# Kernel optimization log

Hardware: AMD Instinct MI355X
Metric: run time of the kernel (lower is better)

The kernel has to match this reference:

```python
import jax, jax.numpy as jnp
import numpy as np


def setup_inputs() -> dict:
    key = jax.random.key(0)
    ks = jax.random.split(key, 8)
    B, C, H, W = 4, 256, 64, 64
    C8 = C // 8
    x = jax.random.normal(ks[0], (B, C, H, W), dtype=jnp.float32)
    # 1x1 conv weights as (out_ch, in_ch) matrices + biases
    Wq = jax.random.normal(ks[1], (C8, C), dtype=jnp.float32) * (1.0 / np.sqrt(C))
    bq = jnp.zeros((C8,), dtype=jnp.float32)
    Wk = jax.random.normal(ks[2], (C8, C), dtype=jnp.float32) * (1.0 / np.sqrt(C))
    bk = jnp.zeros((C8,), dtype=jnp.float32)
    Wv = jax.random.normal(ks[3], (C, C), dtype=jnp.float32) * (1.0 / np.sqrt(C))
    bv = jnp.zeros((C,), dtype=jnp.float32)
    gamma = jax.random.normal(ks[4], (1,), dtype=jnp.float32) * 0.1
    return {"x": x, "Wq": Wq, "bq": bq, "Wk": Wk, "bk": bk, "Wv": Wv, "bv": bv, "gamma": gamma}


def reference(x, Wq, bq, Wk, bk, Wv, bv, gamma):
    B, C, H, W = x.shape
    N = H * W
    xf = x.reshape(B, C, N)  # (B, C, N)
    # 1x1 convs == per-pixel channel matmuls
    q = jnp.einsum('oc,bcn->bon', Wq, xf) + bq[None, :, None]  # (B, C8, N)
    k = jnp.einsum('oc,bcn->bon', Wk, xf) + bk[None, :, None]  # (B, C8, N)
    v = jnp.einsum('oc,bcn->bon', Wv, xf) + bv[None, :, None]  # (B, C, N)
    energy = jnp.einsum('bcn,bcm->bnm', q, k)  # (B, N, N)
    attention = jax.nn.softmax(energy, axis=-1)
    # out[b,c,n] = sum_m v[b,c,m] * attention[b,n,m]
    out = jnp.einsum('bcm,bnm->bcn', v, attention)
    out = out.reshape(B, C, H, W)
    return gamma * out + x
```

## Files before the change

kernel.cpp:

```cpp
#include <hip/hip_runtime.h>
#include <hip/hip_bf16.h>
#include <cstddef>
#include <cstdint>

#define CCH 256
#define DQK 32
#define NPX 4096
#define BQ2 128
#define BM  64
#define NB  4

typedef __attribute__((ext_vector_type(8))) short bf16x8;
typedef __attribute__((ext_vector_type(4))) float f32x4;
typedef __attribute__((ext_vector_type(4))) unsigned int u32x4;

#if __has_builtin(__builtin_amdgcn_exp2f)
#define EXP2F(x) __builtin_amdgcn_exp2f(x)
#else
#define EXP2F(x) exp2f(x)
#endif

__device__ inline unsigned short f2bf(float f) {
    unsigned u = __builtin_bit_cast(unsigned, f);
    u += 0x7FFFu + ((u >> 16) & 1u);
    return (unsigned short)(u >> 16);
}
__device__ inline float bf2f(unsigned short h) {
    unsigned u = (unsigned)h << 16;
    return __builtin_bit_cast(float, u);
}
__device__ inline unsigned pkbf(float a, float b) {
    __hip_bfloat162 h = __float22bfloat162_rn(make_float2(a, b));
    unsigned u;
    __builtin_memcpy(&u, &h, 4);
    return u;
}

__global__ __launch_bounds__(256) void convert_kernel(
    const float* __restrict__ Wq, const float* __restrict__ bq,
    const float* __restrict__ Wk, const float* __restrict__ bk,
    const float* __restrict__ Wv, const float* __restrict__ bv,
    unsigned short* __restrict__ Wb, float* __restrict__ bb)
{
    const float LOG2E = 1.4426950408889634f;
    const int o = blockIdx.x;
    const int c = threadIdx.x;
    float v;
    if (o < 32)       v = Wq[o * CCH + c] * LOG2E;
    else if (o < 64)  v = Wk[(o - 32) * CCH + c];
    else              v = Wv[(o - 64) * CCH + c];
    Wb[o * CCH + c] = f2bf(v);
    if (c == 0)
        bb[o] = (o < 32) ? bq[o] * LOG2E : (o < 64) ? bk[o - 32] : bv[o - 64];
}

__global__ __launch_bounds__(512) void proj_mfma(
    const float* __restrict__ x,
    const unsigned short* __restrict__ Wb, const float* __restrict__ bb,
    unsigned short* __restrict__ ws)
{
    __shared__ __align__(16) unsigned short xT[64][264];

    const int tid  = threadIdx.x;
    const int lane = tid & 63;
    const int w    = tid >> 6;
    const int ln   = lane & 15;
    const int g    = lane >> 4;
    const int bid  = blockIdx.x;

    const int xcd  = bid & 7;
    const int idx  = bid >> 3;
    const int slab = xcd + 8 * (idx / 5);
    const int ocg  = idx % 5;
    const int b    = slab >> 6;
    const int pxt  = slab & 63;
    const int pxg0 = pxt * 64;

    const int mt    = w >> 1;
    const int ocrow = ocg * 64 + mt * 16 + ln;
    bf16x8 a[8];
#pragma unroll
    for (int k8 = 0; k8 < 8; ++k8)
        a[k8] = *(const bf16x8*)(Wb + (size_t)ocrow * CCH + k8 * 32 + g * 8);

    {
        const int pxl = (tid & 15) * 4;
        const int c0  = (tid >> 4) * 8;
        float4 xv[8];
#pragma unroll
        for (int cc = 0; cc < 8; ++cc)
            xv[cc] = *(const float4*)(x + ((size_t)(b * CCH + c0 + cc)) * NPX + pxg0 + pxl);
#pragma unroll
        for (int j = 0; j < 4; ++j) {
            unsigned u[4];
#pragma unroll
            for (int h = 0; h < 4; ++h) {
                const float f0 = ((const float*)&xv[2 * h])[j];
                const float f1 = ((const float*)&xv[2 * h + 1])[j];
                u[h] = pkbf(f0, f1);
            }
            *(u32x4*)&xT[pxl + j][c0] = (u32x4){u[0], u[1], u[2], u[3]};
        }
    }
    __syncthreads();

    const int nt0 = (w & 1) * 2;
    const float4 bb4 = *(const float4*)(bb + ocg * 64 + mt * 16 + g * 4);
    f32x4 acc0 = (f32x4){bb4.x, bb4.y, bb4.z, bb4.w};
    f32x4 acc1 = acc0;
#pragma unroll
    for (int k8 = 0; k8 < 8; ++k8) {
        const bf16x8 b0 = *(const bf16x8*)&xT[nt0 * 16 + ln][k8 * 32 + g * 8];
        const bf16x8 b1 = *(const bf16x8*)&xT[nt0 * 16 + 16 + ln][k8 * 32 + g * 8];
        acc0 = __builtin_amdgcn_mfma_f32_16x16x32_bf16(a[k8], b0, acc0, 0, 0, 0);
        acc1 = __builtin_amdgcn_mfma_f32_16x16x32_bf16(a[k8], b1, acc1, 0, 0, 0);
    }

    unsigned short* qT = ws;
    unsigned short* kT = ws + (size_t)NB * NPX * 32;
    unsigned short* vb = ws + (size_t)2 * NB * NPX * 32;
#pragma unroll
    for (int j = 0; j < 2; ++j) {
        const f32x4 acc = j ? acc1 : acc0;
        const int px = pxg0 + (nt0 + j) * 16 + ln;
        if (ocg == 0) {
            const unsigned lo = pkbf(acc[0], acc[1]);
            const unsigned hi = pkbf(acc[2], acc[3]);
            unsigned short* dst = (mt < 2)
                ? qT + ((size_t)b * NPX + px) * 32 + mt * 16 + g * 4
                : kT + ((size_t)b * NPX + px) * 32 + (mt - 2) * 16 + g * 4;
            *(uint2*)dst = make_uint2(lo, hi);
        } else {
            const int c_row = (ocg - 1) * 64 + mt * 16 + g * 4;
#pragma unroll
            for (int rr = 0; rr < 4; ++rr)
                vb[((size_t)(b * CCH + c_row + rr)) * NPX + px] = f2bf(acc[rr]);
        }
    }
}

__global__ __launch_bounds__(512, 4) void attn_kernel(
    const unsigned short* __restrict__ qT, const unsigned short* __restrict__ kT,
    const unsigned short* __restrict__ vB, const float* __restrict__ x,
    const float* __restrict__ gamma, float* __restrict__ out,
    unsigned short* __restrict__ opart, float* __restrict__ mlm,
    float* __restrict__ mll, int ns)
{
    __shared__ __align__(16) unsigned short Pl[2][BQ2 * 64];
    __shared__ float scb[2][BQ2];
    __shared__ int   flg[2][8];
    __shared__ float l_lds[BQ2];

    const int tid  = threadIdx.x;
    const int lane = tid & 63;
    const int w    = tid >> 6;
    const int ln   = lane & 15;
    const int g    = lane >> 4;
    const int bid  = blockIdx.x;

    const int b    = (bid & 7) >> 1;
    const int jb   = ((bid >> 3) << 1) | (bid & 1);
    const int tile = jb / ns;
    const int s    = jb - tile * ns;
    const int n0   = tile * BQ2;

    const bf16x8 qf = *(const bf16x8*)(qT + ((size_t)b * NPX + n0 + w * 16 + ln) * 32 + g * 8);

    f32x4 acc[8][2];
#pragma unroll
    for (int qt = 0; qt < 8; ++qt) {
        acc[qt][0] = (f32x4){0.f, 0.f, 0.f, 0.f};
        acc[qt][1] = (f32x4){0.f, 0.f, 0.f, 0.f};
    }
    float mreg = -INFINITY, lreg = 0.f;

    const unsigned short* kTb = kT + (size_t)b * NPX * 32;
    const unsigned short* vb  = vB + ((size_t)b * CCH + w * 32) * NPX;
    const int kbase = s * (NPX / ns);
    const int iters = NPX / (ns * BM);
    const unsigned swz   = ((unsigned)ln & 7u) << 4;
    const unsigned myrow = (unsigned)(w * 16 + ln) * 128u;
    const float THR2 = 11.544655f;

    for (int t = 0; t < iters; ++t) {
        const int m0 = kbase + t * BM;

        f32x4 e[4];
#pragma unroll
        for (int s4 = 0; s4 < 4; ++s4) {
            const bf16x8 ka = *(const bf16x8*)(kTb + (size_t)(m0 + s4 * 16 + ln) * 32 + g * 8);
            e[s4] = __builtin_amdgcn_mfma_f32_16x16x32_bf16(
                        ka, qf, (f32x4){0.f, 0.f, 0.f, 0.f}, 0, 0, 0);
        }

        float lm = -INFINITY;
#pragma unroll
        for (int s4 = 0; s4 < 4; ++s4)
#pragma unroll
            for (int rr = 0; rr < 4; ++rr) lm = fmaxf(lm, e[s4][rr]);
        lm = fmaxf(lm, __shfl_xor(lm, 16));
        lm = fmaxf(lm, __shfl_xor(lm, 32));
        const float mnew = (lm <= mreg + THR2) ? mreg : lm;
        const float sc   = EXP2F(mreg - mnew);
        float ps = 0.f;
#pragma unroll
        for (int s4 = 0; s4 < 4; ++s4)
#pragma unroll
            for (int rr = 0; rr < 4; ++rr) {
                const float p = EXP2F(e[s4][rr] - mnew);
                e[s4][rr] = p;
                ps += p;
            }
        ps += __shfl_xor(ps, 16);
        ps += __shfl_xor(ps, 32);
        lreg = lreg * sc + ps;
        mreg = mnew;

        const int bw = t & 1;
        char* const pwb = (char*)&Pl[bw][0];
#pragma unroll
        for (int s4 = 0; s4 < 4; ++s4) {
            uint2 pk;
            pk.x = pkbf(e[s4][0], e[s4][1]);
            pk.y = pkbf(e[s4][2], e[s4][3]);
            *(uint2*)(pwb + myrow + (((unsigned)(s4 * 32 + g * 8)) ^ swz)) = pk;
        }
        if (g == 0) scb[bw][w * 16 + ln] = sc;
        const int allsk = __all(sc == 1.0f);
        if (lane == 0) flg[bw][w] = allsk;

        bf16x8 va[2][2];
#pragma unroll
        for (int ct = 0; ct < 2; ++ct) {
            const unsigned short* vrow = vb + (size_t)(ct * 16 + ln) * NPX + m0 + g * 8;
            va[ct][0] = *(const bf16x8*)(vrow);
            va[ct][1] = *(const bf16x8*)(vrow + 32);
        }

        asm volatile("s_waitcnt lgkmcnt(0)" ::: "memory");
        __builtin_amdgcn_s_barrier();

        int sk = flg[bw][0];
#pragma unroll
        for (int i = 1; i < 8; ++i) sk &= flg[bw][i];
        if (!sk) {
#pragma unroll
            for (int qt = 0; qt < 8; ++qt) {
                const float scq = scb[bw][qt * 16 + ln];
#pragma unroll
                for (int rr = 0; rr < 4; ++rr) {
                    acc[qt][0][rr] *= scq;
                    acc[qt][1][rr] *= scq;
                }
            }
        }
#pragma unroll
        for (int qt = 0; qt < 8; ++qt) {
            const unsigned rb = (unsigned)(qt * 16 + ln) * 128u;
            const bf16x8 pf0 = *(const bf16x8*)(pwb + rb + (((unsigned)(g * 16))      ^ swz));
            const bf16x8 pf1 = *(const bf16x8*)(pwb + rb + (((unsigned)(64 + g * 16)) ^ swz));
            acc[qt][0] = __builtin_amdgcn_mfma_f32_16x16x32_bf16(va[0][0], pf0, acc[qt][0], 0, 0, 0);
            acc[qt][0] = __builtin_amdgcn_mfma_f32_16x16x32_bf16(va[0][1], pf1, acc[qt][0], 0, 0, 0);
            acc[qt][1] = __builtin_amdgcn_mfma_f32_16x16x32_bf16(va[1][0], pf0, acc[qt][1], 0, 0, 0);
            acc[qt][1] = __builtin_amdgcn_mfma_f32_16x16x32_bf16(va[1][1], pf1, acc[qt][1], 0, 0, 0);
        }
    }

    if (opart) {
        const size_t sb = (size_t)(s * NB + b);
#pragma unroll
        for (int qt = 0; qt < 8; ++qt)
#pragma unroll
            for (int ct = 0; ct < 2; ++ct) {
                const size_t c0 = sb * CCH + w * 32 + ct * 16 + g * 4;
#pragma unroll
                for (int rr = 0; rr < 4; ++rr)
                    opart[(c0 + rr) * NPX + n0 + qt * 16 + ln] = f2bf(acc[qt][ct][rr]);
            }
        if (g == 0) {
            mlm[sb * NPX + n0 + w * 16 + ln] = mreg;
            mll[sb * NPX + n0 + w * 16 + ln] = lreg;
        }
    } else {
        if (g == 0) l_lds[w * 16 + ln] = lreg;
        __syncthreads();
        const float gm = gamma[0];
#pragma unroll
        for (int qt = 0; qt < 8; ++qt) {
            const float iv = 1.f / l_lds[qt * 16 + ln];
#pragma unroll
            for (int ct = 0; ct < 2; ++ct) {
                const size_t c0 = (size_t)b * CCH + w * 32 + ct * 16 + g * 4;
#pragma unroll
                for (int rr = 0; rr < 4; ++rr) {
                    const size_t idx = (c0 + rr) * NPX + n0 + qt * 16 + ln;
                    out[idx] = gm * acc[qt][ct][rr] * iv + x[idx];
                }
            }
        }
    }
}

__global__ __launch_bounds__(256) void combine_kernel(
    const unsigned short* __restrict__ opart,
    const float* __restrict__ mlm, const float* __restrict__ mll,
    const float* __restrict__ x, const float* __restrict__ gamma,
    float* __restrict__ out, int ns)
{
    const int idx = blockIdx.x * 256 + threadIdx.x;
    const int bc  = idx >> 9;
    const int b   = bc / CCH;
    const int c   = bc - b * CCH;
    const int n0  = (idx & 511) * 8;

    float M[8];
#pragma unroll
    for (int i = 0; i < 8; ++i) M[i] = -INFINITY;
    for (int s = 0; s < ns; ++s) {
        const float* mp = mlm + ((size_t)(s * NB + b)) * NPX + n0;
#pragma unroll
        for (int i = 0; i < 8; ++i) M[i] = fmaxf(M[i], mp[i]);
    }

    float L[8], O[8];
#pragma unroll
    for (int i = 0; i < 8; ++i) { L[i] = 0.f; O[i] = 0.f; }
    for (int s = 0; s < ns; ++s) {
        const size_t sb = (size_t)(s * NB + b);
        const float* mp = mlm + sb * NPX + n0;
        const float* lp = mll + sb * NPX + n0;
        const bf16x8 v8 = *(const bf16x8*)(opart + (sb * CCH + c) * NPX + n0);
#pragma unroll
        for (int i = 0; i < 8; ++i) {
            const float wgt = EXP2F(mp[i] - M[i]);
            L[i] += wgt * lp[i];
            O[i] += wgt * bf2f((unsigned short)v8[i]);
        }
    }

    const float gm = gamma[0];
    const size_t xo = (size_t)bc * NPX + n0;
    float4 r0, r1;
    const float4 x0 = *(const float4*)(x + xo);
    const float4 x1 = *(const float4*)(x + xo + 4);
    r0.x = gm * O[0] / L[0] + x0.x;  r0.y = gm * O[1] / L[1] + x0.y;
    r0.z = gm * O[2] / L[2] + x0.z;  r0.w = gm * O[3] / L[3] + x0.w;
    r1.x = gm * O[4] / L[4] + x1.x;  r1.y = gm * O[5] / L[5] + x1.y;
    r1.z = gm * O[6] / L[6] + x1.z;  r1.w = gm * O[7] / L[7] + x1.w;
    *(float4*)(out + xo)     = r0;
    *(float4*)(out + xo + 4) = r1;
}

extern "C" void kernel_launch(void* const* d_in, const int* in_sizes, int n_in,
                              void* d_out, int out_size, void* d_ws, size_t ws_size,
                              hipStream_t stream)
{
    const float* x  = (const float*)d_in[0];
    const float* Wq = (const float*)d_in[1];
    const float* bq = (const float*)d_in[2];
    const float* Wk = (const float*)d_in[3];
    const float* bk = (const float*)d_in[4];
    const float* Wv = (const float*)d_in[5];
    const float* bv = (const float*)d_in[6];
    const float* gm = (const float*)d_in[7];
    float* out = (float*)d_out;
    unsigned short* ws = (unsigned short*)d_ws;

    const size_t WB_U16 = 320 * CCH;
    const size_t BB_U16 = 320 * 2;
    const size_t qkvU   = (size_t)2 * NB * NPX * 32 + (size_t)NB * CCH * NPX;
    const size_t qkvB   = (qkvU + WB_U16 + BB_U16) * 2;
    const size_t partB  = (size_t)NB * CCH * NPX * 2;
    const size_t mlB    = (size_t)2 * NB * NPX * 4;
    int ns = 1;
    if      (ws_size >= qkvB + 4 * (partB + mlB)) ns = 4;
    else if (ws_size >= qkvB + 2 * (partB + mlB)) ns = 2;

    unsigned short* Wb = ws + qkvU;
    float*          bb = (float*)(ws + qkvU + WB_U16);

    convert_kernel<<<320, 256, 0, stream>>>(Wq, bq, Wk, bk, Wv, bv, Wb, bb);

    proj_mfma<<<1280, 512, 0, stream>>>(x, Wb, bb, ws);

    const unsigned short* qT = ws;
    const unsigned short* kT = ws + (size_t)NB * NPX * 32;
    const unsigned short* vB = ws + (size_t)2 * NB * NPX * 32;

    const int ablocks = NB * (NPX / BQ2) * ns;

    if (ns > 1) {
        unsigned short* opart = ws + qkvU + WB_U16 + BB_U16;
        float* mlm = (float*)(opart + (size_t)ns * NB * CCH * NPX);
        float* mll = mlm + (size_t)ns * NB * NPX;

        attn_kernel<<<ablocks, 512, 0, stream>>>(qT, kT, vB, x, gm, out,
                                                 opart, mlm, mll, ns);

        const int cblocks = (NB * CCH * (NPX / 8)) / 256;
        combine_kernel<<<cblocks, 256, 0, stream>>>(opart, mlm, mll, x, gm, out, ns);
    } else {
        attn_kernel<<<ablocks, 512, 0, stream>>>(qT, kT, vB, x, gm, out,
                                                 nullptr, nullptr, nullptr, 1);
    }
}
```

Baseline: 91.68 us.

## Widen attention tile to 256 queries with 16 waves and LDS-staged K

Doubles the query tile per block from 128 to 256 and launches 1024 threads (16 waves), each wave now owning 16 output channels instead of 32, so each V fragment load feeds twice as many query tiles. K tiles are now prefetched into a double-buffered LDS area with global_load_lds instead of being read directly from global memory by every wave. This halves the block count and raises per-wave accumulator count. It also risks lower occupancy from the 1024-thread launch bound and larger LDS footprint, and depends on the vmcnt accounting staying correct.

Measured after the change: 92.73 us. About the same (+1.1%).

```diff
diff --git a/kernel.cpp b/kernel.cpp
--- a/kernel.cpp
+++ b/kernel.cpp
@@ -6,9 +6,10 @@
 #define CCH 256
 #define DQK 32
 #define NPX 4096
-#define BQ2 128
+#define BQK 256
 #define BM  64
 #define NB  4
+#define NW  16
 
 typedef __attribute__((ext_vector_type(8))) short bf16x8;
 typedef __attribute__((ext_vector_type(4))) float f32x4;
@@ -139,17 +140,18 @@
     }
 }
 
-__global__ __launch_bounds__(512, 4) void attn_kernel(
+__global__ __launch_bounds__(1024, 4) void attn_kernel(
     const unsigned short* __restrict__ qT, const unsigned short* __restrict__ kT,
     const unsigned short* __restrict__ vB, const float* __restrict__ x,
     const float* __restrict__ gamma, float* __restrict__ out,
     unsigned short* __restrict__ opart, float* __restrict__ mlm,
     float* __restrict__ mll, int ns)
 {
-    __shared__ __align__(16) unsigned short Pl[2][BQ2 * 64];
-    __shared__ float scb[2][BQ2];
-    __shared__ int   flg[2][8];
-    __shared__ float l_lds[BQ2];
+    __shared__ __align__(16) unsigned short Pl[2][BQK * 64];
+    __shared__ __align__(16) unsigned short Kl[2][64 * 32];
+    __shared__ float scb[2][BQK];
+    __shared__ int   flg[2][NW];
+    __shared__ float l_lds[BQK];
 
     const int tid  = threadIdx.x;
     const int lane = tid & 63;
@@ -162,33 +164,49 @@
     const int jb   = ((bid >> 3) << 1) | (bid & 1);
     const int tile = jb / ns;
     const int s    = jb - tile * ns;
-    const int n0   = tile * BQ2;
+    const int n0   = tile * BQK;
 
     const bf16x8 qf = *(const bf16x8*)(qT + ((size_t)b * NPX + n0 + w * 16 + ln) * 32 + g * 8);
 
-    f32x4 acc[8][2];
-#pragma unroll
-    for (int qt = 0; qt < 8; ++qt) {
-        acc[qt][0] = (f32x4){0.f, 0.f, 0.f, 0.f};
-        acc[qt][1] = (f32x4){0.f, 0.f, 0.f, 0.f};
-    }
+    f32x4 acc[16];
+#pragma unroll
+    for (int qt = 0; qt < 16; ++qt) acc[qt] = (f32x4){0.f, 0.f, 0.f, 0.f};
     float mreg = -INFINITY, lreg = 0.f;
 
     const unsigned short* kTb = kT + (size_t)b * NPX * 32;
-    const unsigned short* vb  = vB + ((size_t)b * CCH + w * 32) * NPX;
+    const unsigned short* vb  = vB + ((size_t)b * CCH + w * 16) * NPX;
     const int kbase = s * (NPX / ns);
     const int iters = NPX / (ns * BM);
     const unsigned swz   = ((unsigned)ln & 7u) << 4;
     const unsigned myrow = (unsigned)(w * 16 + ln) * 128u;
     const float THR2 = 11.544655f;
 
+    if (w < 4) {
+        const unsigned short* ksrc = kTb + (size_t)kbase * 32 + w * 512 + lane * 8;
+        __builtin_amdgcn_global_load_lds(
+            (const __attribute__((address_space(1))) void*)ksrc,
+            (__attribute__((address_space(3))) void*)&Kl[0][w * 512], 16, 0, 0);
+    }
+    asm volatile("s_waitcnt vmcnt(0)" ::: "memory");
+    __syncthreads();
+
     for (int t = 0; t < iters; ++t) {
         const int m0 = kbase + t * BM;
-
+        const int mnext = (t + 1 < iters) ? (m0 + BM) : m0;
+        const int nbuf = (t + 1) & 1;
+
+        if (w < 4) {
+            const unsigned short* ksrc = kTb + (size_t)mnext * 32 + w * 512 + lane * 8;
+            __builtin_amdgcn_global_load_lds(
+                (const __attribute__((address_space(1))) void*)ksrc,
+                (__attribute__((address_space(3))) void*)&Kl[nbuf][w * 512], 16, 0, 0);
+        }
+
+        const unsigned short* kl = &Kl[t & 1][0];
         f32x4 e[4];
 #pragma unroll
         for (int s4 = 0; s4 < 4; ++s4) {
-            const bf16x8 ka = *(const bf16x8*)(kTb + (size_t)(m0 + s4 * 16 + ln) * 32 + g * 8);
+            const bf16x8 ka = *(const bf16x8*)(kl + (s4 * 16 + ln) * 32 + g * 8);
             e[s4] = __builtin_amdgcn_mfma_f32_16x16x32_bf16(
                         ka, qf, (f32x4){0.f, 0.f, 0.f, 0.f}, 0, 0, 0);
         }
@@ -229,54 +247,43 @@
         const int allsk = __all(sc == 1.0f);
         if (lane == 0) flg[bw][w] = allsk;
 
-        bf16x8 va[2][2];
-#pragma unroll
-        for (int ct = 0; ct < 2; ++ct) {
-            const unsigned short* vrow = vb + (size_t)(ct * 16 + ln) * NPX + m0 + g * 8;
-            va[ct][0] = *(const bf16x8*)(vrow);
-            va[ct][1] = *(const bf16x8*)(vrow + 32);
-        }
-
-        asm volatile("s_waitcnt lgkmcnt(0)" ::: "memory");
+        const unsigned short* vrow = vb + (size_t)ln * NPX + m0 + g * 8;
+        bf16x8 va0 = *(const bf16x8*)(vrow);
+        bf16x8 va1 = *(const bf16x8*)(vrow + 32);
+
+        asm volatile("s_waitcnt vmcnt(2) lgkmcnt(0)" ::: "memory");
         __builtin_amdgcn_s_barrier();
 
         int sk = flg[bw][0];
 #pragma unroll
-        for (int i = 1; i < 8; ++i) sk &= flg[bw][i];
+        for (int i = 1; i < NW; ++i) sk &= flg[bw][i];
         if (!sk) {
 #pragma unroll
-            for (int qt = 0; qt < 8; ++qt) {
+            for (int qt = 0; qt < 16; ++qt) {
                 const float scq = scb[bw][qt * 16 + ln];
 #pragma unroll
-                for (int rr = 0; rr < 4; ++rr) {
-                    acc[qt][0][rr] *= scq;
-                    acc[qt][1][rr] *= scq;
-                }
+                for (int rr = 0; rr < 4; ++rr) acc[qt][rr] *= scq;
             }
         }
 #pragma unroll
-        for (int qt = 0; qt < 8; ++qt) {
+        for (int qt = 0; qt < 16; ++qt) {
             const unsigned rb = (unsigned)(qt * 16 + ln) * 128u;
             const bf16x8 pf0 = *(const bf16x8*)(pwb + rb + (((unsigned)(g * 16))      ^ swz));
             const bf16x8 pf1 = *(const bf16x8*)(pwb + rb + (((unsigned)(64 + g * 16)) ^ swz));
-            acc[qt][0] = __builtin_amdgcn_mfma_f32_16x16x32_bf16(va[0][0], pf0, acc[qt][0], 0, 0, 0);
-            acc[qt][0] = __builtin_amdgcn_mfma_f32_16x16x32_bf16(va[0][1], pf1, acc[qt][0], 0, 0, 0);
-            acc[qt][1] = __builtin_amdgcn_mfma_f32_16x16x32_bf16(va[1][0], pf0, acc[qt][1], 0, 0, 0);
-            acc[qt][1] = __builtin_amdgcn_mfma_f32_16x16x32_bf16(va[1][1], pf1, acc[qt][1], 0, 0, 0);
+            acc[qt] = __builtin_amdgcn_mfma_f32_16x16x32_bf16(va0, pf0, acc[qt], 0, 0, 0);
+            acc[qt] = __builtin_amdgcn_mfma_f32_16x16x32_bf16(va1, pf1, acc[qt], 0, 0, 0);
         }
     }
 
     if (opart) {
         const size_t sb = (size_t)(s * NB + b);
 #pragma unroll
-        for (int qt = 0; qt < 8; ++qt)
-#pragma unroll
-            for (int ct = 0; ct < 2; ++ct) {
-                const size_t c0 = sb * CCH + w * 32 + ct * 16 + g * 4;
-#pragma unroll
-                for (int rr = 0; rr < 4; ++rr)
-                    opart[(c0 + rr) * NPX + n0 + qt * 16 + ln] = f2bf(acc[qt][ct][rr]);
-            }
+        for (int qt = 0; qt < 16; ++qt) {
+            const size_t c0 = sb * CCH + w * 16 + g * 4;
+#pragma unroll
+            for (int rr = 0; rr < 4; ++rr)
+                opart[(c0 + rr) * NPX + n0 + qt * 16 + ln] = f2bf(acc[qt][rr]);
+        }
         if (g == 0) {
             mlm[sb * NPX + n0 + w * 16 + ln] = mreg;
             mll[sb * NPX + n0 + w * 16 + ln] = lreg;
@@ -286,16 +293,13 @@
         __syncthreads();
         const float gm = gamma[0];
 #pragma unroll
-        for (int qt = 0; qt < 8; ++qt) {
+        for (int qt = 0; qt < 16; ++qt) {
             const float iv = 1.f / l_lds[qt * 16 + ln];
-#pragma unroll
-            for (int ct = 0; ct < 2; ++ct) {
-                const size_t c0 = (size_t)b * CCH + w * 32 + ct * 16 + g * 4;
-#pragma unroll
-                for (int rr = 0; rr < 4; ++rr) {
-                    const size_t idx = (c0 + rr) * NPX + n0 + qt * 16 + ln;
-                    out[idx] = gm * acc[qt][ct][rr] * iv + x[idx];
-                }
+            const size_t c0 = (size_t)b * CCH + w * 16 + g * 4;
+#pragma unroll
+            for (int rr = 0; rr < 4; ++rr) {
+                const size_t idx = (c0 + rr) * NPX + n0 + qt * 16 + ln;
+                out[idx] = gm * acc[qt][rr] * iv + x[idx];
             }
         }
     }
@@ -387,20 +391,20 @@
     const unsigned short* kT = ws + (size_t)NB * NPX * 32;
     const unsigned short* vB = ws + (size_t)2 * NB * NPX * 32;
 
-    const int ablocks = NB * (NPX / BQ2) * ns;
+    const int ablocks = NB * (NPX / BQK) * ns;
 
     if (ns > 1) {
         unsigned short* opart = ws + qkvU + WB_U16 + BB_U16;
         float* mlm = (float*)(opart + (size_t)ns * NB * CCH * NPX);
         float* mll = mlm + (size_t)ns * NB * NPX;
 
-        attn_kernel<<<ablocks, 512, 0, stream>>>(qT, kT, vB, x, gm, out,
-                                                 opart, mlm, mll, ns);
+        attn_kernel<<<ablocks, 1024, 0, stream>>>(qT, kT, vB, x, gm, out,
+                                                  opart, mlm, mll, ns);
 
         const int cblocks = (NB * CCH * (NPX / 8)) / 256;
         combine_kernel<<<cblocks, 256, 0, stream>>>(opart, mlm, mll, x, gm, out, ns);
     } else {
-        attn_kernel<<<ablocks, 512, 0, stream>>>(qT, kT, vB, x, gm, out,
-                                                 nullptr, nullptr, nullptr, 1);
-    }
-}
+        attn_kernel<<<ablocks, 1024, 0, stream>>>(qT, kT, vB, x, gm, out,
+                                                  nullptr, nullptr, nullptr, 1);
+    }
+}
```
